# Performance work log

Hardware: AMD Instinct MI355X
Metric: run time of the kernel (lower is better)

Reference implementation:

```python
import jax, jax.numpy as jnp
import numpy as np


def _gelu(x):
    # torch F.gelu default = exact (erf) gelu
    return jax.nn.gelu(x, approximate=False)


def _gatv2(x, src, dst, Wl, bl, Wr, br, att, bout, n):
    """PyG GATv2Conv, concat=False (mean over heads), negative_slope=0.2."""
    H, C = att.shape
    xl = (x @ Wl + bl).reshape(n, H, C)  # source-side transform (messages)
    xr = (x @ Wr + br).reshape(n, H, C)  # target-side transform
    e = jax.nn.leaky_relu(xl[src] + xr[dst], 0.2)      # [E,H,C]
    logits = jnp.einsum('ehc,hc->eh', e, att)          # [E,H]
    # segment softmax over incoming edges of each target node
    m = jax.ops.segment_max(logits, dst, num_segments=n)
    m = jnp.where(jnp.isfinite(m), m, 0.0)
    p = jnp.exp(logits - m[dst])
    den = jax.ops.segment_sum(p, dst, num_segments=n)
    alpha = p / (den[dst] + 1e-16)
    out = jax.ops.segment_sum(alpha[:, :, None] * xl[src], dst, num_segments=n)  # [N,H,C]
    return out.mean(axis=1) + bout


def _gnorm(x, w, b, ms):
    """PyG GraphNorm with a single graph (batch == zeros)."""
    mu = x.mean(axis=0, keepdims=True)
    o = x - ms * mu
    var = (o * o).mean(axis=0, keepdims=True)
    return w * o / jnp.sqrt(var + 1e-5) + b


def setup_inputs() -> dict:
    N, E, HID, LAT = 50000, 300000, 128, 256
    key = jax.random.key(0)
    ks = iter(jax.random.split(key, 48))

    def rn(shape, s=0.05):
        return jax.random.normal(next(ks), shape, jnp.float32) * s

    d = {}
    d['z_g'] = rn((1, LAT), 1.0)
    d['edge_index'] = jax.random.randint(next(ks), (2, E), 0, N, dtype=jnp.int32)
    d['template_vertices'] = rn((N, 3), 1.0)
    d['W_ne1'] = rn((3, HID)); d['b_ne1'] = jnp.zeros((HID,))
    d['W_ne2'] = rn((HID, HID)); d['b_ne2'] = jnp.zeros((HID,))
    d['W_s1'] = rn((LAT, HID)); d['b_s1'] = jnp.zeros((HID,))
    d['W_s2'] = rn((HID, HID)); d['b_s2'] = jnp.zeros((HID,))
    for i, h in ((1, 2), (2, 2), (3, 1)):
        d[f'Wl{i}'] = rn((HID, h * HID)); d[f'bl{i}'] = jnp.zeros((h * HID,))
        d[f'Wr{i}'] = rn((HID, h * HID)); d[f'br{i}'] = jnp.zeros((h * HID,))
        d[f'att{i}'] = rn((h, HID)); d[f'bo{i}'] = jnp.zeros((HID,))
        d[f'gn{i}_w'] = jnp.ones((HID,)); d[f'gn{i}_b'] = jnp.zeros((HID,))
        d[f'gn{i}_ms'] = jnp.ones((HID,))
    d['W_h1'] = rn((HID, HID // 2)); d['b_h1'] = jnp.zeros((HID // 2,))
    d['W_h2'] = rn((HID // 2, 3)); d['b_h2'] = jnp.zeros((3,))
    return d


def reference(z_g, edge_index, template_vertices,
              W_ne1, b_ne1, W_ne2, b_ne2, W_s1, b_s1, W_s2, b_s2,
              Wl1, bl1, Wr1, br1, att1, bo1, gn1_w, gn1_b, gn1_ms,
              Wl2, bl2, Wr2, br2, att2, bo2, gn2_w, gn2_b, gn2_ms,
              Wl3, bl3, Wr3, br3, att3, bo3, gn3_w, gn3_b, gn3_ms,
              W_h1, b_h1, W_h2, b_h2):
    n = template_vertices.shape[0]
    sl = jnp.arange(n, dtype=edge_index.dtype)
    src = jnp.concatenate([edge_index[0], sl])  # GATv2Conv add_self_loops=True
    dst = jnp.concatenate([edge_index[1], sl])
    # node embedding + broadcast style (eval mode -> dropout is identity)
    x = _gelu(template_vertices @ W_ne1 + b_ne1) @ W_ne2 + b_ne2
    style = _gelu(z_g @ W_s1 + b_s1) @ W_s2 + b_s2   # [1, hidden]
    x = x + style
    x = _gelu(_gnorm(_gatv2(x, src, dst, Wl1, bl1, Wr1, br1, att1, bo1, n), gn1_w, gn1_b, gn1_ms))
    x = _gelu(_gnorm(_gatv2(x, src, dst, Wl2, bl2, Wr2, br2, att2, bo2, n), gn2_w, gn2_b, gn2_ms))
    x = _gelu(_gnorm(_gatv2(x, src, dst, Wl3, bl3, Wr3, br3, att3, bo3, n), gn3_w, gn3_b, gn3_ms))
    displacement = _gelu(x @ W_h1 + b_h1) @ W_h2 + b_h2   # [n, 3]
    return displacement
```

## Files before the change

### kernel.cpp

```cpp
#include <hip/hip_runtime.h>
#include <hip/hip_fp16.h>
#include <math.h>

#define DEVINL __device__ __forceinline__

using bf16x8 = __attribute__((ext_vector_type(8))) short;
using f32x4  = __attribute__((ext_vector_type(4))) float;
using u16x4  = __attribute__((ext_vector_type(4))) unsigned short;
using f16x2  = __attribute__((ext_vector_type(2))) _Float16;

DEVINL float gelu_f(float v) { return 0.5f * v * (1.0f + erff(v * 0.7071067811865475f)); }
DEVINL unsigned short f2bf(float f) {
    union { float f; unsigned u; } c; c.f = f;
    unsigned r = c.u + 0x7fffu + ((c.u >> 16) & 1u);
    return (unsigned short)(r >> 16);
}
DEVINL float bf2f(unsigned short s) {
    union { unsigned u; float f; } c; c.u = (unsigned)s << 16;
    return c.f;
}
DEVINL unsigned short f2h(float f) {
    __half h = __float2half_rn(f);
    return *(unsigned short*)&h;
}
DEVINL f16x2 b2h2(unsigned u) {
    union { unsigned u; f16x2 h; } c; c.u = u; return c.h;
}
DEVINL void gl_lds16(const void* g, void* l) {
    __builtin_amdgcn_global_load_lds(
        (const __attribute__((address_space(1))) unsigned*)g,
        (__attribute__((address_space(3))) unsigned*)l, 16, 0, 0);
}

__global__ void style_k(const float* __restrict__ zg, const float* __restrict__ W1,
                        const float* __restrict__ b1, const float* __restrict__ W2,
                        const float* __restrict__ b2, float* __restrict__ style) {
    __shared__ float s1[128];
    int j = threadIdx.x;
    float a = b1[j];
    for (int k = 0; k < 256; k++) a = fmaf(zg[k], W1[k * 128 + j], a);
    s1[j] = gelu_f(a);
    __syncthreads();
    float o = b2[j];
    for (int k = 0; k < 128; k++) o = fmaf(s1[k], W2[k * 128 + j], o);
    style[j] = o;
}

__global__ void ne1_k(const float* __restrict__ tv, const float* __restrict__ W,
                      const float* __restrict__ b, float* __restrict__ h1,
                      int* __restrict__ counts, int Nn) {
    int idx = blockIdx.x * blockDim.x + threadIdx.x;
    if (idx < Nn) counts[idx] = 0;
    if (idx >= Nn * 128) return;
    int n = idx >> 7, c = idx & 127;
    float o = fmaf(tv[n * 3 + 0], W[c],
              fmaf(tv[n * 3 + 1], W[128 + c],
              fmaf(tv[n * 3 + 2], W[256 + c], b[c])));
    h1[idx] = gelu_f(o);
}

struct PrepArgs {
    const float* src[8];
    unsigned short* dst;
    int dstoff[8];
    int off[9];
    int shift[8];
};
__global__ void prep_k(PrepArgs a) {
    int idx = blockIdx.x * 256 + threadIdx.x;
    if (idx >= a.off[8]) return;
    int s = 0;
    while (idx >= a.off[s + 1]) s++;
    int e = idx - a.off[s];
    int sh = a.shift[s];
    int k = e >> sh, j = e & ((1 << sh) - 1);
    float w = a.src[s][e];
    unsigned short hi = f2bf(w);
    unsigned short lo = f2bf(w - bf2f(hi));
    int c = j >> 4, lr = j & 15;
    int s2 = k >> 5, lk = (k >> 3) & 3, i = k & 7;
    int lane = lk * 16 + lr;
    size_t base = (size_t)a.dstoff[s] + (size_t)c * 4096 + s2 * 512 + lane * 8 + i;
    a.dst[base] = hi;
    a.dst[base + 2048] = lo;
}

template <int OUT, int EPI, bool DUAL, typename OutT, int PRE>
__global__ __launch_bounds__(256) void mfma_lin_k(
    const float* __restrict__ xin,
    const unsigned short* __restrict__ WT0, const float* __restrict__ b0,
    const unsigned short* __restrict__ WT1, const float* __restrict__ b1,
    const float* __restrict__ style, const float* __restrict__ AB,
    OutT* __restrict__ out0, OutT* __restrict__ out1, int Nn) {
    constexpr int CPM = OUT / 16;
    constexpr int NCH = (DUAL ? 2 : 1) * CPM;
    __shared__ uint4 buf[2][512];
    int t = threadIdx.x;
    int wave = t >> 6, lane = t & 63;
    int lr = lane & 15, lk = lane >> 4;
    int base = blockIdx.x * 128 + wave * 32;
    int r0 = base + lr, r1 = base + 16 + lr;
    int cr0 = min(r0, Nn - 1), cr1 = min(r1, Nn - 1);
    const float* px0 = xin + (size_t)cr0 * 128;
    const float* px1 = xin + (size_t)cr1 * 128;

    bf16x8 xh[2][4], xlo[2][4];
#pragma unroll
    for (int s = 0; s < 4; s++) {
        int cb = s * 32 + lk * 8;
        float A_[8], B_[8];
        if constexpr (PRE == 2) {
            *(f32x4*)&A_[0] = *(const f32x4*)(AB + cb);
            *(f32x4*)&A_[4] = *(const f32x4*)(AB + cb + 4);
            *(f32x4*)&B_[0] = *(const f32x4*)(AB + 128 + cb);
            *(f32x4*)&B_[4] = *(const f32x4*)(AB + 128 + cb + 4);
        }
#pragma unroll
        for (int rr = 0; rr < 2; rr++) {
            const float4* p4 = (const float4*)((rr ? px1 : px0) + cb);
            float4 a = p4[0], b = p4[1];
            float v[8] = {a.x, a.y, a.z, a.w, b.x, b.y, b.z, b.w};
            if constexpr (PRE == 2) {
#pragma unroll
                for (int i = 0; i < 8; i++) v[i] = gelu_f(fmaf(A_[i], v[i], B_[i]));
            }
            bf16x8 h, l;
#pragma unroll
            for (int i = 0; i < 8; i++) {
                unsigned short hb = f2bf(v[i]);
                h[i] = (short)hb;
                l[i] = (short)f2bf(v[i] - bf2f(hb));
            }
            xh[rr][s] = h;
            xlo[rr][s] = l;
        }
    }

    auto stage = [&](int c, int bsel) {
        const unsigned short* Wt = (DUAL && c >= CPM) ? WT1 : WT0;
        int cc = (DUAL && c >= CPM) ? c - CPM : c;
        const char* g = (const char*)(Wt + (size_t)cc * 4096);
        char* l = (char*)&buf[bsel][0];
        gl_lds16(g + t * 16, l + wave * 1024);
        gl_lds16(g + 4096 + t * 16, l + 4096 + wave * 1024);
    };

    stage(0, 0);
    for (int c = 0; c < NCH; ++c) {
        int cur = c & 1;
        bool pre = (c + 1 < NCH);
        if (pre) stage(c + 1, cur ^ 1);
        if (pre) asm volatile("s_waitcnt vmcnt(2)" ::: "memory");
        else     asm volatile("s_waitcnt vmcnt(0)" ::: "memory");
        __builtin_amdgcn_s_barrier();

        int m = (DUAL && c >= CPM) ? 1 : 0;
        int j0 = (c - m * CPM) * 16;
        const float* bias = m ? b1 : b0;
        OutT* out = m ? out1 : out0;
        const bf16x8* W = (const bf16x8*)&buf[cur][0];

        f32x4 acc0 = {0.f, 0.f, 0.f, 0.f}, acc1 = {0.f, 0.f, 0.f, 0.f};
#pragma unroll
        for (int s = 0; s < 4; ++s) {
            bf16x8 wh = W[s * 64 + lane];
            bf16x8 wl = W[256 + s * 64 + lane];
            acc0 = __builtin_amdgcn_mfma_f32_16x16x32_bf16(wh, xh[0][s], acc0, 0, 0, 0);
            acc0 = __builtin_amdgcn_mfma_f32_16x16x32_bf16(wh, xlo[0][s], acc0, 0, 0, 0);
            acc0 = __builtin_amdgcn_mfma_f32_16x16x32_bf16(wl, xh[0][s], acc0, 0, 0, 0);
            acc1 = __builtin_amdgcn_mfma_f32_16x16x32_bf16(wh, xh[1][s], acc1, 0, 0, 0);
            acc1 = __builtin_amdgcn_mfma_f32_16x16x32_bf16(wh, xlo[1][s], acc1, 0, 0, 0);
            acc1 = __builtin_amdgcn_mfma_f32_16x16x32_bf16(wl, xh[1][s], acc1, 0, 0, 0);
        }
        int j = j0 + lk * 4;
        float o0[4], o1[4];
#pragma unroll
        for (int i = 0; i < 4; i++) {
            float bb = bias[j + i];
            if (EPI == 1) bb += style[j + i];
            float v0 = acc0[i] + bb, v1 = acc1[i] + bb;
            if (EPI == 2) { v0 = gelu_f(v0); v1 = gelu_f(v1); }
            o0[i] = v0; o1[i] = v1;
        }
        if constexpr (sizeof(OutT) == 2) {
            u16x4 s0 = {f2h(o0[0]), f2h(o0[1]), f2h(o0[2]), f2h(o0[3])};
            u16x4 s1v = {f2h(o1[0]), f2h(o1[1]), f2h(o1[2]), f2h(o1[3])};
            if (r0 < Nn) *(u16x4*)((unsigned short*)out + (size_t)r0 * OUT + j) = s0;
            if (r1 < Nn) *(u16x4*)((unsigned short*)out + (size_t)r1 * OUT + j) = s1v;
        } else {
            if (r0 < Nn) { f32x4 v = {o0[0], o0[1], o0[2], o0[3]}; *(f32x4*)((float*)out + (size_t)r0 * OUT + j) = v; }
            if (r1 < Nn) { f32x4 v = {o1[0], o1[1], o1[2], o1[3]}; *(f32x4*)((float*)out + (size_t)r1 * OUT + j) = v; }
        }
        __builtin_amdgcn_s_barrier();
    }
}

__global__ void count_k(const int* __restrict__ dst, int* __restrict__ counts, int E, int EP) {
    int e = blockIdx.x * blockDim.x + threadIdx.x;
    if (e >= EP) return;
    int d = (e < E) ? dst[e] : (e - E);
    atomicAdd(&counts[d], 1);
}

__global__ void tile_sum_k(const int* __restrict__ counts, int* __restrict__ tsum, int Nn) {
    int i = blockIdx.x * 256 + threadIdx.x;
    int v = (i < Nn) ? counts[i] : 0;
    int lane = threadIdx.x & 63, wave = threadIdx.x >> 6;
#pragma unroll
    for (int off = 1; off < 64; off <<= 1) v += __shfl_xor(v, off, 64);
    __shared__ int red[4];
    if (lane == 0) red[wave] = v;
    __syncthreads();
    if (threadIdx.x == 0) tsum[blockIdx.x] = red[0] + red[1] + red[2] + red[3];
}

__global__ void tile_scan_k(const int* __restrict__ tsum, int* __restrict__ toff,
                            int ntiles, int* __restrict__ rowptr, int Nn, int total) {
    __shared__ int s[256];
    int t = threadIdx.x;
    int v = (t < ntiles) ? tsum[t] : 0;
    s[t] = v;
    __syncthreads();
    for (int off = 1; off < 256; off <<= 1) {
        int a = (t >= off) ? s[t - off] : 0;
        __syncthreads();
        s[t] += a;
        __syncthreads();
    }
    if (t < ntiles) toff[t] = s[t] - v;
    if (t == 0) rowptr[Nn] = total;
}

__global__ void tile_write_k(const int* __restrict__ counts, const int* __restrict__ toff,
                             int* __restrict__ rowptr, int* __restrict__ fillc, int Nn) {
    int i = blockIdx.x * 256 + threadIdx.x;
    int t = threadIdx.x;
    int v = (i < Nn) ? counts[i] : 0;
    if (i < Nn) fillc[i] = 0;
    __shared__ int s[256];
    s[t] = v;
    __syncthreads();
    for (int off = 1; off < 256; off <<= 1) {
        int a = (t >= off) ? s[t - off] : 0;
        __syncthreads();
        s[t] += a;
        __syncthreads();
    }
    if (i < Nn) rowptr[i] = toff[blockIdx.x] + s[t] - v;
}

__global__ void fill_k(const int* __restrict__ src, const int* __restrict__ dst,
                       const int* __restrict__ rowptr, int* __restrict__ fillc,
                       int* __restrict__ col, int E, int EP) {
    int e = blockIdx.x * blockDim.x + threadIdx.x;
    if (e >= EP) return;
    int d = (e < E) ? dst[e] : (e - E);
    int s = (e < E) ? src[e] : (e - E);
    int pos = atomicAdd(&fillc[d], 1);
    col[rowptr[d] + pos] = s;
}

template <int H>
__global__ __launch_bounds__(256) void gat_gather_k(
    const unsigned short* __restrict__ xl, const unsigned short* __restrict__ xr,
    const float* __restrict__ att, const float* __restrict__ bo,
    const int* __restrict__ rowptr, const int* __restrict__ col,
    float* __restrict__ y, float* __restrict__ stats, int Nn) {
    if (blockIdx.x == 0 && threadIdx.x < 256) stats[threadIdx.x] = 0.f;
    constexpr int NPB = (H == 2) ? 2 : 4;
    int w = threadIdx.x >> 6;
    int slot = (H == 2) ? (w >> 1) : w;
    int h = (H == 2) ? (w & 1) : 0;
    int lane = threadIdx.x & 63;
    int g = lane >> 4, sub = lane & 15;
    constexpr int HC = H * 128;
    int n = blockIdx.x * NPB + slot;
    bool act = n < Nn;
    int nn = act ? n : 0;

    uint4 uxr = *(const uint4*)(xr + (size_t)nn * HC + h * 128 + sub * 8);
    f16x2 xrv[4] = {b2h2(uxr.x), b2h2(uxr.y), b2h2(uxr.z), b2h2(uxr.w)};
    const float* ap = att + h * 128 + sub * 8;
    f16x2 a2[4];
#pragma unroll
    for (int i = 0; i < 4; i++) {
        f16x2 t; t.x = (_Float16)ap[2 * i]; t.y = (_Float16)ap[2 * i + 1];
        a2[i] = t;
    }
    f16x2 c02; c02.x = (_Float16)0.2f; c02.y = (_Float16)0.2f;

    float den = 0.f;
    float acc[8] = {0.f, 0.f, 0.f, 0.f, 0.f, 0.f, 0.f, 0.f};
    int beg = act ? rowptr[n] : 0, endp = act ? rowptr[n + 1] : 0;

    for (int k0 = beg; k0 < endp; k0 += 4) {
        int k = k0 + g;
        bool ev = k < endp;
        int s = col[ev ? k : beg];
        uint4 u = *(const uint4*)(xl + (size_t)s * HC + h * 128 + sub * 8);
        f16x2 v2[4] = {b2h2(u.x), b2h2(u.y), b2h2(u.z), b2h2(u.w)};
        float p = 0.f;
#pragma unroll
        for (int i = 0; i < 4; i++) {
            f16x2 t = v2[i] + xrv[i];
            f16x2 e = __builtin_elementwise_max(t, t * c02);
#if __has_builtin(__builtin_amdgcn_fdot2)
            p = __builtin_amdgcn_fdot2(e, a2[i], p, false);
#else
            p = fmaf((float)e.x, (float)a2[i].x, p);
            p = fmaf((float)e.y, (float)a2[i].y, p);
#endif
        }
        p += __shfl_xor(p, 1, 64);
        p += __shfl_xor(p, 2, 64);
        p += __shfl_xor(p, 4, 64);
        p += __shfl_xor(p, 8, 64);
        float pe = ev ? __expf(p) : 0.f;
        den += pe;
#pragma unroll
        for (int i = 0; i < 4; i++) {
            acc[2 * i]     = fmaf(pe, (float)v2[i].x, acc[2 * i]);
            acc[2 * i + 1] = fmaf(pe, (float)v2[i].y, acc[2 * i + 1]);
        }
    }
#pragma unroll
    for (int off = 16; off <= 32; off <<= 1) {
        den += __shfl_xor(den, off, 64);
#pragma unroll
        for (int j = 0; j < 8; j++) acc[j] += __shfl_xor(acc[j], off, 64);
    }
    float inv = 1.0f / (den + 1e-16f);

    if constexpr (H == 1) {
        if (act && g == 0) {
            const float* bp = bo + sub * 8;
            f32x4 o0 = {acc[0] * inv + bp[0], acc[1] * inv + bp[1], acc[2] * inv + bp[2], acc[3] * inv + bp[3]};
            f32x4 o1 = {acc[4] * inv + bp[4], acc[5] * inv + bp[5], acc[6] * inv + bp[6], acc[7] * inv + bp[7]};
            *(f32x4*)(y + (size_t)n * 128 + sub * 8) = o0;
            *(f32x4*)(y + (size_t)n * 128 + sub * 8 + 4) = o1;
        }
    } else {
        __shared__ float sh[NPB][2][128];
        if (g == 0) {
#pragma unroll
            for (int j = 0; j < 8; j++) sh[slot][h][sub * 8 + j] = acc[j] * inv;
        }
        __syncthreads();
        int t = threadIdx.x;
        int slot2 = t >> 7, c = t & 127;
        int n2 = blockIdx.x * NPB + slot2;
        if (n2 < Nn)
            y[(size_t)n2 * 128 + c] = (sh[slot2][0][c] + sh[slot2][1][c]) * 0.5f + bo[c];
    }
}

__global__ void gn_stats_k(const float* __restrict__ y, float* __restrict__ stats, int Nn) {
    int c = threadIdx.x;
    int per = (Nn + gridDim.x - 1) / gridDim.x;
    int n0 = blockIdx.x * per, n1 = min(n0 + per, Nn);
    float s = 0.f, s2 = 0.f;
    for (int n = n0; n < n1; n++) {
        float v = y[(size_t)n * 128 + c];
        s += v;
        s2 = fmaf(v, v, s2);
    }
    atomicAdd(&stats[c], s);
    atomicAdd(&stats[128 + c], s2);
}

__global__ void gn_final_k(const float* __restrict__ stats, const float* __restrict__ w,
                           const float* __restrict__ b, const float* __restrict__ ms,
                           float* __restrict__ AB, float invN) {
    int c = threadIdx.x;
    float mu = stats[c] * invN;
    float ex2 = stats[128 + c] * invN;
    float msv = ms[c];
    float var = ex2 - 2.f * msv * mu * mu + msv * msv * mu * mu;
    float r = rsqrtf(var + 1e-5f);
    float A = w[c] * r;
    AB[c] = A;
    AB[128 + c] = b[c] - A * msv * mu;
}

__global__ void head2_k(const float* __restrict__ h, const float* __restrict__ W,
                        const float* __restrict__ b, float* __restrict__ out, int Nn) {
    __shared__ float w[192];
    __shared__ float bb[3];
    int t = threadIdx.x;
    if (t < 192) w[t] = W[t];
    if (t < 3) bb[t] = b[t];
    __syncthreads();
    int n = blockIdx.x * blockDim.x + t;
    if (n >= Nn) return;
    float a0 = bb[0], a1 = bb[1], a2 = bb[2];
    const float4* h4 = reinterpret_cast<const float4*>(h + (size_t)n * 64);
    for (int k4 = 0; k4 < 16; k4++) {
        float4 v = h4[k4];
        int k = k4 * 4;
        a0 = fmaf(v.x, w[(k + 0) * 3 + 0], a0); a1 = fmaf(v.x, w[(k + 0) * 3 + 1], a1); a2 = fmaf(v.x, w[(k + 0) * 3 + 2], a2);
        a0 = fmaf(v.y, w[(k + 1) * 3 + 0], a0); a1 = fmaf(v.y, w[(k + 1) * 3 + 1], a1); a2 = fmaf(v.y, w[(k + 1) * 3 + 2], a2);
        a0 = fmaf(v.z, w[(k + 2) * 3 + 0], a0); a1 = fmaf(v.z, w[(k + 2) * 3 + 1], a1); a2 = fmaf(v.z, w[(k + 2) * 3 + 2], a2);
        a0 = fmaf(v.w, w[(k + 3) * 3 + 0], a0); a1 = fmaf(v.w, w[(k + 3) * 3 + 1], a1); a2 = fmaf(v.w, w[(k + 3) * 3 + 2], a2);
    }
    out[n * 3 + 0] = a0;
    out[n * 3 + 1] = a1;
    out[n * 3 + 2] = a2;
}

extern "C" void kernel_launch(void* const* d_in, const int* in_sizes, int n_in,
                              void* d_out, int out_size, void* d_ws, size_t ws_size,
                              hipStream_t stream) {
    const float* zg = (const float*)d_in[0];
    const int* ei = (const int*)d_in[1];
    const float* tv = (const float*)d_in[2];
    const float* W_ne1 = (const float*)d_in[3];
    const float* b_ne1 = (const float*)d_in[4];
    const float* W_ne2 = (const float*)d_in[5];
    const float* b_ne2 = (const float*)d_in[6];
    const float* W_s1 = (const float*)d_in[7];
    const float* b_s1 = (const float*)d_in[8];
    const float* W_s2 = (const float*)d_in[9];
    const float* b_s2 = (const float*)d_in[10];
    const float *Wl[3], *bl[3], *Wr[3], *br[3], *attp[3], *bop[3], *gnw[3], *gnb[3], *gnms[3];
    for (int L = 0; L < 3; L++) {
        int base = 11 + L * 9;
        Wl[L] = (const float*)d_in[base + 0];
        bl[L] = (const float*)d_in[base + 1];
        Wr[L] = (const float*)d_in[base + 2];
        br[L] = (const float*)d_in[base + 3];
        attp[L] = (const float*)d_in[base + 4];
        bop[L] = (const float*)d_in[base + 5];
        gnw[L] = (const float*)d_in[base + 6];
        gnb[L] = (const float*)d_in[base + 7];
        gnms[L] = (const float*)d_in[base + 8];
    }
    const float* W_h1 = (const float*)d_in[38];
    const float* b_h1 = (const float*)d_in[39];
    const float* W_h2 = (const float*)d_in[40];
    const float* b_h2 = (const float*)d_in[41];

    int E = in_sizes[1] / 2;
    int N = in_sizes[2] / 3;
    int EP = E + N;
    int NT = (N + 255) / 256;
    const int* srcp = ei;
    const int* dstp = ei + E;

    char* p = (char*)d_ws;
    auto alloc = [&](size_t bytes) -> char* {
        char* r = p;
        p += (bytes + 255) & ~(size_t)255;
        return r;
    };
    float* style = (float*)alloc(512);
    float* h1 = (float*)alloc((size_t)N * 128 * 4);
    float* x = (float*)alloc((size_t)N * 128 * 4);
    unsigned short* xle = (unsigned short*)alloc((size_t)N * 256 * 2);
    unsigned short* xre = (unsigned short*)alloc((size_t)N * 256 * 2);
    float* y = (float*)alloc((size_t)N * 128 * 4);
    float* hb = (float*)alloc((size_t)N * 64 * 4);
    float* stats = (float*)alloc(1024);
    float* AB = (float*)alloc(1024);
    int* rowptr = (int*)alloc(((size_t)N + 1) * 4);
    int* counts = (int*)alloc((size_t)N * 4);
    int* fillc = (int*)alloc((size_t)N * 4);
    int* col = (int*)alloc((size_t)EP * 4);
    int* tsum = (int*)alloc((size_t)NT * 4);
    int* toff = (int*)alloc((size_t)NT * 4);
    unsigned short* wt = (unsigned short*)alloc((size_t)376832 * 2);

    PrepArgs pa;
    const float* srcs[8] = {W_ne2, Wl[0], Wr[0], Wl[1], Wr[1], Wl[2], Wr[2], W_h1};
    int outs[8] = {128, 256, 256, 256, 256, 128, 128, 64};
    int off = 0;
    pa.dst = wt;
    for (int s = 0; s < 8; s++) {
        pa.src[s] = srcs[s];
        pa.off[s] = off;
        pa.dstoff[s] = 2 * off;
        pa.shift[s] = (outs[s] == 256) ? 8 : (outs[s] == 128 ? 7 : 6);
        off += 128 * outs[s];
    }
    pa.off[8] = off;
    const unsigned short* ws_ne2 = wt + pa.dstoff[0];
    const unsigned short* ws_l[3] = {wt + pa.dstoff[1], wt + pa.dstoff[3], wt + pa.dstoff[5]};
    const unsigned short* ws_r[3] = {wt + pa.dstoff[2], wt + pa.dstoff[4], wt + pa.dstoff[6]};
    const unsigned short* ws_h1 = wt + pa.dstoff[7];
    prep_k<<<(off + 255) / 256, 256, 0, stream>>>(pa);

    float invN = 1.0f / (float)N;

    style_k<<<1, 128, 0, stream>>>(zg, W_s1, b_s1, W_s2, b_s2, style);
    ne1_k<<<(N * 128 + 255) / 256, 256, 0, stream>>>(tv, W_ne1, b_ne1, h1, counts, N);
    mfma_lin_k<128, 1, false, float, 0><<<(N + 127) / 128, 256, 0, stream>>>(
        h1, ws_ne2, b_ne2, nullptr, nullptr, style, nullptr, x, nullptr, N);

    count_k<<<(EP + 255) / 256, 256, 0, stream>>>(dstp, counts, E, EP);
    tile_sum_k<<<NT, 256, 0, stream>>>(counts, tsum, N);
    tile_scan_k<<<1, 256, 0, stream>>>(tsum, toff, NT, rowptr, N, EP);
    tile_write_k<<<NT, 256, 0, stream>>>(counts, toff, rowptr, fillc, N);
    fill_k<<<(EP + 255) / 256, 256, 0, stream>>>(srcp, dstp, rowptr, fillc, col, E, EP);

    mfma_lin_k<256, 0, true, unsigned short, 0><<<(N + 127) / 128, 256, 0, stream>>>(
        x, ws_l[0], bl[0], ws_r[0], br[0], nullptr, nullptr, xle, xre, N);
    gat_gather_k<2><<<(N + 1) / 2, 256, 0, stream>>>(xle, xre, attp[0], bop[0], rowptr, col, y, stats, N);
    gn_stats_k<<<512, 128, 0, stream>>>(y, stats, N);
    gn_final_k<<<1, 128, 0, stream>>>(stats, gnw[0], gnb[0], gnms[0], AB, invN);

    mfma_lin_k<256, 0, true, unsigned short, 2><<<(N + 127) / 128, 256, 0, stream>>>(
        y, ws_l[1], bl[1], ws_r[1], br[1], nullptr, AB, xle, xre, N);
    gat_gather_k<2><<<(N + 1) / 2, 256, 0, stream>>>(xle, xre, attp[1], bop[1], rowptr, col, y, stats, N);
    gn_stats_k<<<512, 128, 0, stream>>>(y, stats, N);
    gn_final_k<<<1, 128, 0, stream>>>(stats, gnw[1], gnb[1], gnms[1], AB, invN);

    mfma_lin_k<128, 0, true, unsigned short, 2><<<(N + 127) / 128, 256, 0, stream>>>(
        y, ws_l[2], bl[2], ws_r[2], br[2], nullptr, AB, xle, xre, N);
    gat_gather_k<1><<<(N + 3) / 4, 256, 0, stream>>>(xle, xre, attp[2], bop[2], rowptr, col, y, stats, N);
    gn_stats_k<<<512, 128, 0, stream>>>(y, stats, N);
    gn_final_k<<<1, 128, 0, stream>>>(stats, gnw[2], gnb[2], gnms[2], AB, invN);

    mfma_lin_k<64, 2, false, float, 2><<<(N + 127) / 128, 256, 0, stream>>>(
        y, ws_h1, b_h1, nullptr, nullptr, nullptr, AB, hb, nullptr, N);
    head2_k<<<(N + 255) / 256, 256, 0, stream>>>(hb, W_h2, b_h2, (float*)d_out, N);
}
```

Measured before the change: 607.2 us.

## Split dual linear across grid y and remap H=2 gather to one wave per node

The dual-output MFMA linear kernels now split their output chunks across a second grid dimension, so each block handles half of the Wl/Wr chunks. This doubles the block count, at the cost of each block recomputing the bf16 hi/lo split of its input rows. The two-head GAT gather now gives each node a single wave, with one half-wave per head and two edges per iteration. Heads are combined with cross-lane shuffles instead of shared memory and a block barrier, which removes the LDS round trip but halves edge-level parallelism per node.

```diff
diff --git a/kernel.cpp b/kernel.cpp
--- a/kernel.cpp
+++ b/kernel.cpp
@@ -85,7 +85,7 @@
     a.dst[base + 2048] = lo;
 }
 
-template <int OUT, int EPI, bool DUAL, typename OutT, int PRE>
+template <int OUT, int EPI, bool DUAL, typename OutT, int PRE, int SPLIT>
 __global__ __launch_bounds__(256) void mfma_lin_k(
     const float* __restrict__ xin,
     const unsigned short* __restrict__ WT0, const float* __restrict__ b0,
@@ -94,11 +94,13 @@
     OutT* __restrict__ out0, OutT* __restrict__ out1, int Nn) {
     constexpr int CPM = OUT / 16;
     constexpr int NCH = (DUAL ? 2 : 1) * CPM;
+    constexpr int CPB = NCH / SPLIT;
     __shared__ uint4 buf[2][512];
     int t = threadIdx.x;
     int wave = t >> 6, lane = t & 63;
     int lr = lane & 15, lk = lane >> 4;
     int base = blockIdx.x * 128 + wave * 32;
+    int c0 = blockIdx.y * CPB;
     int r0 = base + lr, r1 = base + 16 + lr;
     int cr0 = min(r0, Nn - 1), cr1 = min(r1, Nn - 1);
     const float* px0 = xin + (size_t)cr0 * 128;
@@ -145,10 +147,11 @@
         gl_lds16(g + 4096 + t * 16, l + 4096 + wave * 1024);
     };
 
-    stage(0, 0);
-    for (int c = 0; c < NCH; ++c) {
-        int cur = c & 1;
-        bool pre = (c + 1 < NCH);
+    stage(c0, 0);
+    for (int ci = 0; ci < CPB; ++ci) {
+        int c = c0 + ci;
+        int cur = ci & 1;
+        bool pre = (ci + 1 < CPB);
         if (pre) stage(c + 1, cur ^ 1);
         if (pre) asm volatile("s_waitcnt vmcnt(2)" ::: "memory");
         else     asm volatile("s_waitcnt vmcnt(0)" ::: "memory");
@@ -260,25 +263,19 @@
     col[rowptr[d] + pos] = s;
 }
 
-template <int H>
-__global__ __launch_bounds__(256) void gat_gather_k(
+__global__ __launch_bounds__(256) void gat2_k(
     const unsigned short* __restrict__ xl, const unsigned short* __restrict__ xr,
     const float* __restrict__ att, const float* __restrict__ bo,
     const int* __restrict__ rowptr, const int* __restrict__ col,
     float* __restrict__ y, float* __restrict__ stats, int Nn) {
     if (blockIdx.x == 0 && threadIdx.x < 256) stats[threadIdx.x] = 0.f;
-    constexpr int NPB = (H == 2) ? 2 : 4;
-    int w = threadIdx.x >> 6;
-    int slot = (H == 2) ? (w >> 1) : w;
-    int h = (H == 2) ? (w & 1) : 0;
+    int n = blockIdx.x * 4 + (threadIdx.x >> 6);
     int lane = threadIdx.x & 63;
-    int g = lane >> 4, sub = lane & 15;
-    constexpr int HC = H * 128;
-    int n = blockIdx.x * NPB + slot;
+    int h = lane >> 5, grp = (lane >> 4) & 1, sub = lane & 15;
     bool act = n < Nn;
     int nn = act ? n : 0;
 
-    uint4 uxr = *(const uint4*)(xr + (size_t)nn * HC + h * 128 + sub * 8);
+    uint4 uxr = *(const uint4*)(xr + (size_t)nn * 256 + h * 128 + sub * 8);
     f16x2 xrv[4] = {b2h2(uxr.x), b2h2(uxr.y), b2h2(uxr.z), b2h2(uxr.w)};
     const float* ap = att + h * 128 + sub * 8;
     f16x2 a2[4];
@@ -293,11 +290,11 @@
     float acc[8] = {0.f, 0.f, 0.f, 0.f, 0.f, 0.f, 0.f, 0.f};
     int beg = act ? rowptr[n] : 0, endp = act ? rowptr[n + 1] : 0;
 
-    for (int k0 = beg; k0 < endp; k0 += 4) {
-        int k = k0 + g;
+    for (int k0 = beg; k0 < endp; k0 += 2) {
+        int k = k0 + grp;
         bool ev = k < endp;
         int s = col[ev ? k : beg];
-        uint4 u = *(const uint4*)(xl + (size_t)s * HC + h * 128 + sub * 8);
+        uint4 u = *(const uint4*)(xl + (size_t)s * 256 + h * 128 + sub * 8);
         f16x2 v2[4] = {b2h2(u.x), b2h2(u.y), b2h2(u.z), b2h2(u.w)};
         float p = 0.f;
 #pragma unroll
@@ -323,6 +320,82 @@
             acc[2 * i + 1] = fmaf(pe, (float)v2[i].y, acc[2 * i + 1]);
         }
     }
+    den += __shfl_xor(den, 16, 64);
+#pragma unroll
+    for (int j = 0; j < 8; j++) acc[j] += __shfl_xor(acc[j], 16, 64);
+    float inv = 1.0f / (den + 1e-16f);
+    float o[8];
+#pragma unroll
+    for (int j = 0; j < 8; j++) o[j] = acc[j] * inv;
+#pragma unroll
+    for (int j = 0; j < 8; j++) o[j] = (o[j] + __shfl_xor(o[j], 32, 64)) * 0.5f;
+    if (act && lane < 16) {
+        const float* bp = bo + sub * 8;
+        f32x4 w0 = {o[0] + bp[0], o[1] + bp[1], o[2] + bp[2], o[3] + bp[3]};
+        f32x4 w1 = {o[4] + bp[4], o[5] + bp[5], o[6] + bp[6], o[7] + bp[7]};
+        *(f32x4*)(y + (size_t)n * 128 + sub * 8) = w0;
+        *(f32x4*)(y + (size_t)n * 128 + sub * 8 + 4) = w1;
+    }
+}
+
+__global__ __launch_bounds__(256) void gat1_k(
+    const unsigned short* __restrict__ xl, const unsigned short* __restrict__ xr,
+    const float* __restrict__ att, const float* __restrict__ bo,
+    const int* __restrict__ rowptr, const int* __restrict__ col,
+    float* __restrict__ y, float* __restrict__ stats, int Nn) {
+    if (blockIdx.x == 0 && threadIdx.x < 256) stats[threadIdx.x] = 0.f;
+    int w = threadIdx.x >> 6;
+    int lane = threadIdx.x & 63;
+    int g = lane >> 4, sub = lane & 15;
+    int n = blockIdx.x * 4 + w;
+    bool act = n < Nn;
+    int nn = act ? n : 0;
+
+    uint4 uxr = *(const uint4*)(xr + (size_t)nn * 128 + sub * 8);
+    f16x2 xrv[4] = {b2h2(uxr.x), b2h2(uxr.y), b2h2(uxr.z), b2h2(uxr.w)};
+    const float* ap = att + sub * 8;
+    f16x2 a2[4];
+#pragma unroll
+    for (int i = 0; i < 4; i++) {
+        f16x2 t; t.x = (_Float16)ap[2 * i]; t.y = (_Float16)ap[2 * i + 1];
+        a2[i] = t;
+    }
+    f16x2 c02; c02.x = (_Float16)0.2f; c02.y = (_Float16)0.2f;
+
+    float den = 0.f;
+    float acc[8] = {0.f, 0.f, 0.f, 0.f, 0.f, 0.f, 0.f, 0.f};
+    int beg = act ? rowptr[n] : 0, endp = act ? rowptr[n + 1] : 0;
+
+    for (int k0 = beg; k0 < endp; k0 += 4) {
+        int k = k0 + g;
+        bool ev = k < endp;
+        int s = col[ev ? k : beg];
+        uint4 u = *(const uint4*)(xl + (size_t)s * 128 + sub * 8);
+        f16x2 v2[4] = {b2h2(u.x), b2h2(u.y), b2h2(u.z), b2h2(u.w)};
+        float p = 0.f;
+#pragma unroll
+        for (int i = 0; i < 4; i++) {
+            f16x2 t = v2[i] + xrv[i];
+            f16x2 e = __builtin_elementwise_max(t, t * c02);
+#if __has_builtin(__builtin_amdgcn_fdot2)
+            p = __builtin_amdgcn_fdot2(e, a2[i], p, false);
+#else
+            p = fmaf((float)e.x, (float)a2[i].x, p);
+            p = fmaf((float)e.y, (float)a2[i].y, p);
+#endif
+        }
+        p += __shfl_xor(p, 1, 64);
+        p += __shfl_xor(p, 2, 64);
+        p += __shfl_xor(p, 4, 64);
+        p += __shfl_xor(p, 8, 64);
+        float pe = ev ? __expf(p) : 0.f;
+        den += pe;
+#pragma unroll
+        for (int i = 0; i < 4; i++) {
+            acc[2 * i]     = fmaf(pe, (float)v2[i].x, acc[2 * i]);
+            acc[2 * i + 1] = fmaf(pe, (float)v2[i].y, acc[2 * i + 1]);
+        }
+    }
 #pragma unroll
     for (int off = 16; off <= 32; off <<= 1) {
         den += __shfl_xor(den, off, 64);
@@ -330,27 +403,12 @@
         for (int j = 0; j < 8; j++) acc[j] += __shfl_xor(acc[j], off, 64);
     }
     float inv = 1.0f / (den + 1e-16f);
-
-    if constexpr (H == 1) {
-        if (act && g == 0) {
-            const float* bp = bo + sub * 8;
-            f32x4 o0 = {acc[0] * inv + bp[0], acc[1] * inv + bp[1], acc[2] * inv + bp[2], acc[3] * inv + bp[3]};
-            f32x4 o1 = {acc[4] * inv + bp[4], acc[5] * inv + bp[5], acc[6] * inv + bp[6], acc[7] * inv + bp[7]};
-            *(f32x4*)(y + (size_t)n * 128 + sub * 8) = o0;
-            *(f32x4*)(y + (size_t)n * 128 + sub * 8 + 4) = o1;
-        }
-    } else {
-        __shared__ float sh[NPB][2][128];
-        if (g == 0) {
-#pragma unroll
-            for (int j = 0; j < 8; j++) sh[slot][h][sub * 8 + j] = acc[j] * inv;
-        }
-        __syncthreads();
-        int t = threadIdx.x;
-        int slot2 = t >> 7, c = t & 127;
-        int n2 = blockIdx.x * NPB + slot2;
-        if (n2 < Nn)
-            y[(size_t)n2 * 128 + c] = (sh[slot2][0][c] + sh[slot2][1][c]) * 0.5f + bo[c];
+    if (act && g == 0) {
+        const float* bp = bo + sub * 8;
+        f32x4 o0 = {acc[0] * inv + bp[0], acc[1] * inv + bp[1], acc[2] * inv + bp[2], acc[3] * inv + bp[3]};
+        f32x4 o1 = {acc[4] * inv + bp[4], acc[5] * inv + bp[5], acc[6] * inv + bp[6], acc[7] * inv + bp[7]};
+        *(f32x4*)(y + (size_t)n * 128 + sub * 8) = o0;
+        *(f32x4*)(y + (size_t)n * 128 + sub * 8 + 4) = o1;
     }
 }
 
@@ -489,10 +547,11 @@
     prep_k<<<(off + 255) / 256, 256, 0, stream>>>(pa);
 
     float invN = 1.0f / (float)N;
+    int NB = (N + 127) / 128;
 
     style_k<<<1, 128, 0, stream>>>(zg, W_s1, b_s1, W_s2, b_s2, style);
     ne1_k<<<(N * 128 + 255) / 256, 256, 0, stream>>>(tv, W_ne1, b_ne1, h1, counts, N);
-    mfma_lin_k<128, 1, false, float, 0><<<(N + 127) / 128, 256, 0, stream>>>(
+    mfma_lin_k<128, 1, false, float, 0, 1><<<NB, 256, 0, stream>>>(
         h1, ws_ne2, b_ne2, nullptr, nullptr, style, nullptr, x, nullptr, N);
 
     count_k<<<(EP + 255) / 256, 256, 0, stream>>>(dstp, counts, E, EP);
@@ -501,25 +560,25 @@
     tile_write_k<<<NT, 256, 0, stream>>>(counts, toff, rowptr, fillc, N);
     fill_k<<<(EP + 255) / 256, 256, 0, stream>>>(srcp, dstp, rowptr, fillc, col, E, EP);
 
-    mfma_lin_k<256, 0, true, unsigned short, 0><<<(N + 127) / 128, 256, 0, stream>>>(
+    mfma_lin_k<256, 0, true, unsigned short, 0, 2><<<dim3(NB, 2), 256, 0, stream>>>(
         x, ws_l[0], bl[0], ws_r[0], br[0], nullptr, nullptr, xle, xre, N);
-    gat_gather_k<2><<<(N + 1) / 2, 256, 0, stream>>>(xle, xre, attp[0], bop[0], rowptr, col, y, stats, N);
+    gat2_k<<<(N + 3) / 4, 256, 0, stream>>>(xle, xre, attp[0], bop[0], rowptr, col, y, stats, N);
     gn_stats_k<<<512, 128, 0, stream>>>(y, stats, N);
     gn_final_k<<<1, 128, 0, stream>>>(stats, gnw[0], gnb[0], gnms[0], AB, invN);
 
-    mfma_lin_k<256, 0, true, unsigned short, 2><<<(N + 127) / 128, 256, 0, stream>>>(
+    mfma_lin_k<256, 0, true, unsigned short, 2, 2><<<dim3(NB, 2), 256, 0, stream>>>(
         y, ws_l[1], bl[1], ws_r[1], br[1], nullptr, AB, xle, xre, N);
-    gat_gather_k<2><<<(N + 1) / 2, 256, 0, stream>>>(xle, xre, attp[1], bop[1], rowptr, col, y, stats, N);
+    gat2_k<<<(N + 3) / 4, 256, 0, stream>>>(xle, xre, attp[1], bop[1], rowptr, col, y, stats, N);
     gn_stats_k<<<512, 128, 0, stream>>>(y, stats, N);
     gn_final_k<<<1, 128, 0, stream>>>(stats, gnw[1], gnb[1], gnms[1], AB, invN);
 
-    mfma_lin_k<128, 0, true, unsigned short, 2><<<(N + 127) / 128, 256, 0, stream>>>(
+    mfma_lin_k<128, 0, true, unsigned short, 2, 2><<<dim3(NB, 2), 256, 0, stream>>>(
         y, ws_l[2], bl[2], ws_r[2], br[2], nullptr, AB, xle, xre, N);
-    gat_gather_k<1><<<(N + 3) / 4, 256, 0, stream>>>(xle, xre, attp[2], bop[2], rowptr, col, y, stats, N);
+    gat1_k<<<(N + 3) / 4, 256, 0, stream>>>(xle, xre, attp[2], bop[2], rowptr, col, y, stats, N);
     gn_stats_k<<<512, 128, 0, stream>>>(y, stats, N);
     gn_final_k<<<1, 128, 0, stream>>>(stats, gnw[2], gnb[2], gnms[2], AB, invN);
 
-    mfma_lin_k<64, 2, false, float, 2><<<(N + 127) / 128, 256, 0, stream>>>(
+    mfma_lin_k<64, 2, false, float, 2, 1><<<NB, 256, 0, stream>>>(
         y, ws_h1, b_h1, nullptr, nullptr, nullptr, AB, hb, nullptr, N);
     head2_k<<<(N + 255) / 256, 256, 0, stream>>>(hb, W_h2, b_h2, (float*)d_out, N);
 }
```

New measurement: 607.1 us. Within noise of the previous version (-0.0%).
